# Kernel tuning notes

Hardware: AMD Instinct MI355X
Metric: run time of the kernel (lower is better)

Reference implementation:

```python
import jax, jax.numpy as jnp
import numpy as np

B, N, A = 32, 1024, 256          # batch, n_entities, n_agents
D_IN, D_H, H = 256, 256, 8       # input_dim, hidden_dim, n_heads
SCALE = 1.0 / np.sqrt(D_H)
EPS = 1e-12


def setup_inputs() -> dict:
    key = jax.random.key(0)
    ks = jax.random.split(key, 7)
    x = jax.random.normal(ks[0], (B, N, D_IN), dtype=jnp.float32)
    # binary visibility mask [batch, n_agents, n_entities]
    m = (jax.random.uniform(ks[1], (B, A, N)) > 0.5).astype(jnp.float32)
    # encoder Linear(input_dim, hidden_dim): weight [out,in], bias [out]
    W_enc = jax.random.normal(ks[2], (D_H, D_IN), dtype=jnp.float32) / np.sqrt(D_IN)
    b_enc = jnp.zeros((D_H,), dtype=jnp.float32)
    # per-head projection matrices stacked [H, D_H, D_H] (torch.randn init)
    WQ = jax.random.normal(ks[3], (H, D_H, D_H), dtype=jnp.float32)
    WK = jax.random.normal(ks[4], (H, D_H, D_H), dtype=jnp.float32)
    WV = jax.random.normal(ks[5], (H, D_H, D_H), dtype=jnp.float32)
    return {"x": x, "m": m, "W_enc": W_enc, "b_enc": b_enc, "WQ": WQ, "WK": WK, "WV": WV}


def reference(x, m, W_enc, b_enc, WQ, WK, WV):
    # encode: LeakyReLU then Linear
    h = jnp.einsum('bni,oi->bno', jax.nn.leaky_relu(x), W_enc) + b_enc  # [B,N,D_H]
    n_agents = m.shape[1]
    ha = h[:, :n_agents]                                   # [B,A,D_H]
    # per-head projections, heads vectorized
    Q = jnp.einsum('bad,hde->bhae', ha, WQ)                # [B,H,A,D_H]
    K = jnp.einsum('bnd,hde->bhne', h, WK)                 # [B,H,N,D_H]
    V = jnp.einsum('bnd,hde->bhne', h, WV)                 # [B,H,N,D_H]
    S = jnp.einsum('bhae,bhne->bhan', Q, K) * SCALE        # [B,H,A,N]
    P = jax.nn.softmax(S, axis=-1)
    P = P * m[:, None]                                     # post-softmax mask
    prob = P / (jnp.sum(P, axis=-1, keepdims=True) + EPS)  # renormalize
    z = jnp.einsum('bhan,bhne->bhae', prob, V)             # [B,H,A,D_H]
    return jnp.mean(z, axis=1)                             # [B,A,D_H]
```

## Files before the change

kernel.cpp:

```cpp
#include <hip/hip_runtime.h>
#include <math.h>

namespace {
constexpr int B_N  = 32;
constexpr int SEQ  = 1024;
constexpr int AG   = 256;
constexpr int D    = 256;
constexpr int NH   = 8;
constexpr float SCALE = 0.0625f;
constexpr float EPS   = 1e-12f;

constexpr size_t HHI_OFF  = 0;
constexpr size_t HLO_OFF  = 16777216;
constexpr size_t HT_OFF   = 33554432;
constexpr size_t MTHI_OFF = 50331648;
constexpr size_t MTLO_OFF = 51380224;
constexpr size_t MB_OFF   = 52428800;
constexpr size_t WVT_OFF  = 53477376;
constexpr size_t Z16_OFF  = 54525952;
}

typedef __attribute__((ext_vector_type(8))) short short8;
typedef __attribute__((ext_vector_type(4))) float floatx4;
#define MFMA_BF(A,B,C) __builtin_amdgcn_mfma_f32_16x16x32_bf16(A,B,C,0,0,0)

__device__ __forceinline__ unsigned short bf16_rtne(float f) {
    unsigned u = __float_as_uint(f);
    u += 0x7fffu + ((u >> 16) & 1u);
    return (unsigned short)(u >> 16);
}
__device__ __forceinline__ float bf16_tof(unsigned short h) {
    return __uint_as_float(((unsigned)h) << 16);
}
__device__ __forceinline__ void async16(void* lds, const void* g) {
    __builtin_amdgcn_global_load_lds(
        (const __attribute__((address_space(1))) unsigned int*)g,
        (__attribute__((address_space(3))) unsigned int*)lds,
        16, 0, 0);
}

__global__ __launch_bounds__(256) void enc_kernel(
    const float* __restrict__ x, const float* __restrict__ W_enc,
    const float* __restrict__ b_enc,
    ushort* __restrict__ h_hi, ushort* __restrict__ h_lo)
{
    __shared__ float AsT[32][68];
    __shared__ float BsT[32][68];
    const int t  = threadIdx.x;
    const int tx = t & 15, ty = t >> 4;
    const int col0 = blockIdx.x * 64;
    const int row0 = blockIdx.y * 64;

    float acc[4][4];
#pragma unroll
    for (int r = 0; r < 4; ++r)
#pragma unroll
        for (int c = 0; c < 4; ++c) acc[r][c] = 0.f;

    for (int k0 = 0; k0 < 256; k0 += 32) {
        __syncthreads();
#pragma unroll
        for (int ss = 0; ss < 2; ++ss) {
            int flat = t + 256 * ss;
            int rr = flat >> 3, k4 = flat & 7;
            float4 v = *(const float4*)(x + (size_t)(row0 + rr) * 256 + k0 + k4 * 4);
            v.x = v.x > 0.f ? v.x : 0.01f * v.x;
            v.y = v.y > 0.f ? v.y : 0.01f * v.y;
            v.z = v.z > 0.f ? v.z : 0.01f * v.z;
            v.w = v.w > 0.f ? v.w : 0.01f * v.w;
            AsT[k4*4+0][rr] = v.x; AsT[k4*4+1][rr] = v.y;
            AsT[k4*4+2][rr] = v.z; AsT[k4*4+3][rr] = v.w;
            float4 wv = *(const float4*)(W_enc + (size_t)(col0 + rr) * 256 + k0 + k4 * 4);
            BsT[k4*4+0][rr] = wv.x; BsT[k4*4+1][rr] = wv.y;
            BsT[k4*4+2][rr] = wv.z; BsT[k4*4+3][rr] = wv.w;
        }
        __syncthreads();
#pragma unroll 8
        for (int kk = 0; kk < 32; ++kk) {
            float4 a4 = *(const float4*)&AsT[kk][ty * 4];
            float4 b4 = *(const float4*)&BsT[kk][tx * 4];
            const float ar[4] = {a4.x, a4.y, a4.z, a4.w};
            const float bc[4] = {b4.x, b4.y, b4.z, b4.w};
#pragma unroll
            for (int r = 0; r < 4; ++r)
#pragma unroll
                for (int c = 0; c < 4; ++c)
                    acc[r][c] = fmaf(ar[r], bc[c], acc[r][c]);
        }
    }

    float4 bv = *(const float4*)(b_enc + col0 + tx * 4);
    const float bb4[4] = {bv.x, bv.y, bv.z, bv.w};
#pragma unroll
    for (int r = 0; r < 4; ++r) {
        const int row = row0 + ty * 4 + r;
        ushort hi4[4], lo4[4];
#pragma unroll
        for (int c = 0; c < 4; ++c) {
            float v = acc[r][c] + bb4[c];
            hi4[c] = bf16_rtne(v);
            lo4[c] = bf16_rtne(v - bf16_tof(hi4[c]));
        }
        *(ushort4*)(h_hi + (size_t)row * 256 + col0 + tx * 4) =
            make_ushort4(hi4[0], hi4[1], hi4[2], hi4[3]);
        *(ushort4*)(h_lo + (size_t)row * 256 + col0 + tx * 4) =
            make_ushort4(lo4[0], lo4[1], lo4[2], lo4[3]);
    }
}

__global__ __launch_bounds__(256) void prep_fused(
    const float* __restrict__ m, unsigned* __restrict__ mb,
    const ushort* __restrict__ h_hi, ushort* __restrict__ hT,
    const float* __restrict__ WV, ushort* __restrict__ WVt,
    const float* __restrict__ WQ, const float* __restrict__ WK,
    ushort* __restrict__ Mt_hi, ushort* __restrict__ Mt_lo)
{
    __shared__ __align__(16) char plds[17408];
    const int t = threadIdx.x;
    const int v = blockIdx.x;

    if (v < 1024) {
        const int idx = v * 256 + t;
        const float4* src = (const float4*)(m + (size_t)idx * 32);
        unsigned wbits = 0;
#pragma unroll
        for (int i = 0; i < 8; ++i) {
            float4 vv = src[i];
            wbits |= (vv.x > 0.5f ? 1u : 0u) << (i * 4 + 0);
            wbits |= (vv.y > 0.5f ? 1u : 0u) << (i * 4 + 1);
            wbits |= (vv.z > 0.5f ? 1u : 0u) << (i * 4 + 2);
            wbits |= (vv.w > 0.5f ? 1u : 0u) << (i * 4 + 3);
        }
        mb[idx] = wbits;
    } else if (v < 3072) {
        ushort (*T)[72] = (ushort(*)[72])plds;
        const int v1 = v - 1024;
        const int n0 = (v1 & 15) * 64, d0 = ((v1 >> 4) & 3) * 64, b = v1 >> 6;
        {
            const int r = t >> 2, c = (t & 3) * 16;
            const ushort* src = h_hi + ((size_t)(b * 1024 + n0 + r)) * 256 + d0 + c;
            *(short8*)&T[r][c]     = *(const short8*)src;
            *(short8*)&T[r][c + 8] = *(const short8*)(src + 8);
        }
        __syncthreads();
        {
            const int dd = t >> 2, seg = (t & 3) * 16;
            ushort tmp[16];
#pragma unroll
            for (int j = 0; j < 16; ++j) tmp[j] = T[seg + j][dd];
            ushort* dst = hT + ((size_t)(b * 256 + d0 + dd)) * 1024 + n0 + seg;
            *(short8*)dst       = *(short8*)&tmp[0];
            *(short8*)(dst + 8) = *(short8*)&tmp[8];
        }
    } else if (v < 3200) {
        float (*T)[68] = (float(*)[68])plds;
        const int v2 = v - 3072;
        const int d0 = (v2 & 3) * 64, e0 = ((v2 >> 2) & 3) * 64, h = v2 >> 4;
        {
            const int r = t >> 2, c = (t & 3) * 16;
            const float* src = WV + ((size_t)(h * 256 + d0 + r)) * 256 + e0 + c;
#pragma unroll
            for (int j = 0; j < 4; ++j)
                *(float4*)&T[r][c + j * 4] = *(const float4*)(src + j * 4);
        }
        __syncthreads();
        {
            const int ee = t >> 2, seg = (t & 3) * 16;
            ushort tmp[16];
#pragma unroll
            for (int j = 0; j < 16; ++j) tmp[j] = bf16_rtne(T[seg + j][ee]);
            ushort* dst = WVt + ((size_t)(h * 256 + e0 + ee)) * 256 + d0 + seg;
            *(short8*)dst       = *(short8*)&tmp[0];
            *(short8*)(dst + 8) = *(short8*)&tmp[8];
        }
    } else {
        float (*AsT)[68] = (float(*)[68])plds;
        float (*BsT)[68] = (float(*)[68])(plds + 8704);
        const int v3 = v - 3200;
        const int tx = t & 15, ty = t >> 4;
        const int col0 = (v3 & 3) * 64;
        const int row0 = ((v3 >> 2) & 3) * 64;
        const int hz   = v3 >> 4;
        const float* A  = WK + (size_t)hz * 256 * 256;
        const float* Bm = WQ + (size_t)hz * 256 * 256;
        ushort* Chi = Mt_hi + (size_t)hz * 256 * 256;
        ushort* Clo = Mt_lo + (size_t)hz * 256 * 256;

        float acc[4][4];
#pragma unroll
        for (int r = 0; r < 4; ++r)
#pragma unroll
            for (int c = 0; c < 4; ++c) acc[r][c] = 0.f;

        for (int k0 = 0; k0 < 256; k0 += 32) {
            __syncthreads();
#pragma unroll
            for (int ss = 0; ss < 2; ++ss) {
                int flat = t + 256 * ss;
                int rr = flat >> 3, k4 = flat & 7;
                float4 vv = *(const float4*)(A + (size_t)(row0 + rr) * 256 + k0 + k4 * 4);
                AsT[k4*4+0][rr] = vv.x; AsT[k4*4+1][rr] = vv.y;
                AsT[k4*4+2][rr] = vv.z; AsT[k4*4+3][rr] = vv.w;
                float4 wv = *(const float4*)(Bm + (size_t)(col0 + rr) * 256 + k0 + k4 * 4);
                BsT[k4*4+0][rr] = wv.x; BsT[k4*4+1][rr] = wv.y;
                BsT[k4*4+2][rr] = wv.z; BsT[k4*4+3][rr] = wv.w;
            }
            __syncthreads();
#pragma unroll 8
            for (int kk = 0; kk < 32; ++kk) {
                float4 a4 = *(const float4*)&AsT[kk][ty * 4];
                float4 b4 = *(const float4*)&BsT[kk][tx * 4];
                const float ar[4] = {a4.x, a4.y, a4.z, a4.w};
                const float bc[4] = {b4.x, b4.y, b4.z, b4.w};
#pragma unroll
                for (int r = 0; r < 4; ++r)
#pragma unroll
                    for (int c = 0; c < 4; ++c)
                        acc[r][c] = fmaf(ar[r], bc[c], acc[r][c]);
            }
        }
#pragma unroll
        for (int r = 0; r < 4; ++r) {
            const int row = row0 + ty * 4 + r;
            ushort hi4[4], lo4[4];
#pragma unroll
            for (int c = 0; c < 4; ++c) {
                float vv = acc[r][c];
                hi4[c] = bf16_rtne(vv);
                lo4[c] = bf16_rtne(vv - bf16_tof(hi4[c]));
            }
            *(ushort4*)(Chi + (size_t)row * 256 + col0 + tx * 4) =
                make_ushort4(hi4[0], hi4[1], hi4[2], hi4[3]);
            *(ushort4*)(Clo + (size_t)row * 256 + col0 + tx * 4) =
                make_ushort4(lo4[0], lo4[1], lo4[2], lo4[3]);
        }
    }
}

__global__ __launch_bounds__(512, 2) void attn_mfma(
    const ushort* __restrict__ h_hi, const ushort* __restrict__ h_lo,
    const ushort* __restrict__ hT,   const ushort* __restrict__ Mt_hi,
    const ushort* __restrict__ Mt_lo, const unsigned* __restrict__ mbits,
    ushort* __restrict__ zout)
{
    __shared__ __align__(16) char lds[118784];
    ushort* pP = (ushort*)(lds + 98304);
    ushort* pE = (ushort*)(lds + 108544);

    const int t    = threadIdx.x;
    const int wv   = t >> 6;
    const int lane = t & 63;
    const int l15  = lane & 15;
    const int quad = lane >> 4;
    const int f    = blockIdx.x;
    const int b    = (f & 7) + 8 * (f >> 7);
    const int mid  = (f >> 3) & 15;
    const int hh   = (mid >> 2) * 2 + (wv >> 2);
    const int a0   = (mid & 3) * 64;
    const int aw   = a0 + (wv & 3) * 16;

    const ushort* hbh = h_hi + (size_t)b * SEQ * D;
    const ushort* hbl = h_lo + (size_t)b * SEQ * D;
    const ushort* hTb = hT   + (size_t)b * D * SEQ;

    floatx4 qac[16];
#pragma unroll
    for (int i = 0; i < 16; ++i) qac[i] = (floatx4){0.f, 0.f, 0.f, 0.f};

    for (int kc = 0; kc < 4; ++kc) {
        short8 Ah[2], Al[2];
#pragma unroll
        for (int kt = 0; kt < 2; ++kt) {
            const size_t ao = ((size_t)b * SEQ + aw + l15) * D +
                              kc * 64 + kt * 32 + quad * 8;
            Ah[kt] = *(const short8*)(h_hi + ao);
            Al[kt] = *(const short8*)(h_lo + ao);
        }
#pragma unroll
        for (int nt2 = 0; nt2 < 16; ++nt2) {
#pragma unroll
            for (int kt = 0; kt < 2; ++kt) {
                const size_t mo = ((size_t)hh * D + nt2 * 16 + l15) * D +
                                  kc * 64 + kt * 32 + quad * 8;
                short8 Bh = *(const short8*)(Mt_hi + mo);
                short8 Bl = *(const short8*)(Mt_lo + mo);
                qac[nt2] = MFMA_BF(Ah[kt], Bh, qac[nt2]);
                qac[nt2] = MFMA_BF(Al[kt], Bh, qac[nt2]);
                qac[nt2] = MFMA_BF(Ah[kt], Bl, qac[nt2]);
            }
        }
    }

    short8 Qhi[8], Qlo[8];
    {
        float* qscr = (float*)lds;
        for (int c = 0; c < 4; ++c) {
#pragma unroll
            for (int j = 0; j < 4; ++j)
#pragma unroll
                for (int r = 0; r < 4; ++r)
                    qscr[(wv * 16 + quad * 4 + r) * 68 + j * 16 + l15] = qac[c * 4 + j][r];
#pragma unroll
            for (int kt = 0; kt < 2; ++kt) {
                const float* pr = &qscr[(wv * 16 + l15) * 68 + kt * 32 + quad * 8];
                float ftmp[8];
                *(float4*)&ftmp[0] = *(const float4*)pr;
                *(float4*)&ftmp[4] = *(const float4*)(pr + 4);
                short8 hi, lo;
#pragma unroll
                for (int e = 0; e < 8; ++e) {
                    unsigned short hb = bf16_rtne(ftmp[e]);
                    hi[e] = (short)hb;
                    lo[e] = (short)bf16_rtne(ftmp[e] - bf16_tof(hb));
                }
                Qhi[c * 2 + kt] = hi;
                Qlo[c * 2 + kt] = lo;
            }
        }
    }
    __syncthreads();

    auto issue_tile = [&](char* buf, int n0) {
        ushort* dh = (ushort*)buf;
        ushort* dl = (ushort*)(buf + 16384);
        ushort* dT = (ushort*)(buf + 32768);
#pragma unroll
        for (int i = 0; i < 2; ++i) {
            const int slot = wv * 128 + i * 64 + lane;
            const int row  = slot >> 5;
            const int p    = slot & 31;
            const int c    = p ^ (row & 7);
            const size_t go = (size_t)(n0 + row) * 256 + c * 8;
            const size_t lo_ = (size_t)(wv * 128 + i * 64) * 8;
            async16(dh + lo_, hbh + go);
            async16(dl + lo_, hbl + go);
        }
#pragma unroll
        for (int i = 0; i < 2; ++i) {
            const int slot = wv * 128 + i * 64 + lane;
            const int row  = slot >> 2;
            const int p    = slot & 3;
            const int c    = p ^ ((row >> 2) & 3);
            async16(dT + (size_t)(wv * 128 + i * 64) * 8,
                    hTb + (size_t)row * 1024 + n0 + c * 8);
        }
    };

    issue_tile(lds,         0);
    issue_tile(lds + 49152, 32);
    __syncthreads();

    floatx4 zac[16];
#pragma unroll
    for (int i = 0; i < 16; ++i) zac[i] = (floatx4){0.f, 0.f, 0.f, 0.f};
    floatx4 zacZ = (floatx4){0.f, 0.f, 0.f, 0.f};
    floatx4 zacE = (floatx4){0.f, 0.f, 0.f, 0.f};
    float mx[4] = {-INFINITY, -INFINITY, -INFINITY, -INFINITY};

    short8 onesf;
#pragma unroll
    for (int e = 0; e < 8; ++e) onesf[e] = (short)0x3F80;

    const unsigned* mbr = mbits + ((size_t)b * AG + aw + quad * 4) * (SEQ / 32);

    for (int nt = 0; nt < 32; ++nt) {
        char* cur = lds + (size_t)(nt & 1) * 49152;
        ushort* hS_hi = (ushort*)cur;
        ushort* hS_lo = (ushort*)(cur + 16384);
        ushort* hTS   = (ushort*)(cur + 32768);

        floatx4 sacH[2], sacL[2];
        sacH[0] = (floatx4){0.f, 0.f, 0.f, 0.f};
        sacH[1] = (floatx4){0.f, 0.f, 0.f, 0.f};
        sacL[0] = (floatx4){0.f, 0.f, 0.f, 0.f};
        sacL[1] = (floatx4){0.f, 0.f, 0.f, 0.f};
#pragma unroll
        for (int ks = 0; ks < 8; ++ks) {
            const int cg = ks * 4 + quad;
#pragma unroll
            for (int ntile = 0; ntile < 2; ++ntile) {
                const int row = ntile * 16 + l15;
                const int off = row * 256 + (cg ^ (row & 7)) * 8;
                short8 Bh = *(const short8*)&hS_hi[off];
                short8 Bl = *(const short8*)&hS_lo[off];
                sacH[ntile] = MFMA_BF(Qhi[ks], Bh, sacH[ntile]);
                sacL[ntile] = MFMA_BF(Qlo[ks], Bh, sacL[ntile]);
                sacL[ntile] = MFMA_BF(Qhi[ks], Bl, sacL[ntile]);
            }
        }

        float l0[4], l1[4];
#pragma unroll
        for (int r = 0; r < 4; ++r) {
            l0[r] = (sacH[0][r] + sacL[0][r]) * SCALE;
            l1[r] = (sacH[1][r] + sacL[1][r]) * SCALE;
        }

        float mt[4];
#pragma unroll
        for (int r = 0; r < 4; ++r) mt[r] = fmaxf(l0[r], l1[r]);
#pragma unroll
        for (int off = 1; off < 16; off <<= 1) {
#pragma unroll
            for (int r = 0; r < 4; ++r)
                mt[r] = fmaxf(mt[r], __shfl_xor(mt[r], off));
        }

        const bool need = (mt[0] > mx[0] + 8.0f) || (mt[1] > mx[1] + 8.0f) ||
                          (mt[2] > mx[2] + 8.0f) || (mt[3] > mx[3] + 8.0f);
        if (__any(need)) {
            float alr[4];
#pragma unroll
            for (int r = 0; r < 4; ++r) {
                const float mxn = fmaxf(mx[r], mt[r]);
                alr[r] = __expf(mx[r] - mxn);
                mx[r] = mxn;
            }
#pragma unroll
            for (int dt = 0; dt < 16; ++dt) {
                zac[dt][0] *= alr[0]; zac[dt][1] *= alr[1];
                zac[dt][2] *= alr[2]; zac[dt][3] *= alr[3];
            }
            zacZ[0] *= alr[0]; zacZ[1] *= alr[1];
            zacZ[2] *= alr[2]; zacZ[3] *= alr[3];
            zacE[0] *= alr[0]; zacE[1] *= alr[1];
            zacE[2] *= alr[2]; zacE[3] *= alr[3];
        }

#pragma unroll
        for (int r = 0; r < 4; ++r) {
            const unsigned w0 = mbr[r * (SEQ / 32) + nt];
            const float e0 = __expf(l0[r] - mx[r]);
            const float e1 = __expf(l1[r] - mx[r]);
            const float p0 = ((w0 >> l15) & 1u)        ? e0 : 0.f;
            const float p1 = ((w0 >> (16 + l15)) & 1u) ? e1 : 0.f;
            const int row = wv * 16 + quad * 4 + r;
            pP[row * 40 + l15]      = bf16_rtne(p0);
            pP[row * 40 + 16 + l15] = bf16_rtne(p1);
            pE[row * 40 + l15]      = bf16_rtne(e0);
            pE[row * 40 + 16 + l15] = bf16_rtne(e1);
        }

        short8 Pf = *(const short8*)&pP[(wv * 16 + l15) * 40 + quad * 8];
        short8 Ef = *(const short8*)&pE[(wv * 16 + l15) * 40 + quad * 8];
        zacZ = MFMA_BF(Pf, onesf, zacZ);
        zacE = MFMA_BF(Ef, onesf, zacE);

#pragma unroll
        for (int dt = 0; dt < 16; ++dt) {
            const int row = dt * 16 + l15;
            const int p   = quad ^ ((row >> 2) & 3);
            short8 Bf = *(const short8*)&hTS[row * 32 + p * 8];
            zac[dt] = MFMA_BF(Pf, Bf, zac[dt]);
        }

        __syncthreads();
        if (nt + 2 < 32) issue_tile(cur, (nt + 2) * 32);
    }

#pragma unroll
    for (int r = 0; r < 4; ++r) {
        const int a = aw + quad * 4 + r;
        const float inv = 1.0f / (zacZ[r] + EPS * zacE[r]);
        ushort* zr = zout + (((size_t)b * NH + hh) * AG + a) * D;
#pragma unroll
        for (int dt = 0; dt < 16; ++dt)
            zr[dt * 16 + l15] = bf16_rtne(zac[dt][r] * inv);
    }
}

__global__ __launch_bounds__(256) void out_mfma(
    const ushort* __restrict__ z16, const ushort* __restrict__ WVt,
    float* __restrict__ out)
{
    const int t    = threadIdx.x;
    const int wv   = t >> 6;
    const int lane = t & 63;
    const int l15  = lane & 15;
    const int quad = lane >> 4;
    const int e0 = blockIdx.x * 64;
    const int a0 = blockIdx.y * 64;
    const int b  = blockIdx.z;
    const int aw = a0 + wv * 16;

    floatx4 acc[4];
#pragma unroll
    for (int i = 0; i < 4; ++i) acc[i] = (floatx4){0.f, 0.f, 0.f, 0.f};

#pragma unroll 4
    for (int c = 0; c < 64; ++c) {
        const int hh = c >> 3, d0 = (c & 7) * 32;
        short8 Af = *(const short8*)(z16 +
            (((size_t)b * NH + hh) * AG + aw + l15) * D + d0 + quad * 8);
#pragma unroll
        for (int et = 0; et < 4; ++et) {
            short8 Bf = *(const short8*)(WVt +
                ((size_t)hh * D + e0 + et * 16 + l15) * D + d0 + quad * 8);
            acc[et] = MFMA_BF(Af, Bf, acc[et]);
        }
    }
#pragma unroll
    for (int et = 0; et < 4; ++et)
#pragma unroll
        for (int r = 0; r < 4; ++r)
            out[((size_t)b * AG + aw + quad * 4 + r) * D + e0 + et * 16 + l15] =
                acc[et][r] * 0.125f;
}

extern "C" void kernel_launch(void* const* d_in, const int* in_sizes, int n_in,
                              void* d_out, int out_size, void* d_ws, size_t ws_size,
                              hipStream_t stream)
{
    (void)in_sizes; (void)n_in; (void)out_size; (void)ws_size;
    const float* x     = (const float*)d_in[0];
    const float* m     = (const float*)d_in[1];
    const float* W_enc = (const float*)d_in[2];
    const float* b_enc = (const float*)d_in[3];
    const float* WQ    = (const float*)d_in[4];
    const float* WK    = (const float*)d_in[5];
    const float* WV    = (const float*)d_in[6];
    float* out = (float*)d_out;
    char* ws = (char*)d_ws;

    ushort*   h_hi  = (ushort*)(ws + HHI_OFF);
    ushort*   h_lo  = (ushort*)(ws + HLO_OFF);
    ushort*   hT    = (ushort*)(ws + HT_OFF);
    ushort*   Mt_hi = (ushort*)(ws + MTHI_OFF);
    ushort*   Mt_lo = (ushort*)(ws + MTLO_OFF);
    unsigned* mbits = (unsigned*)(ws + MB_OFF);
    ushort*   WVt   = (ushort*)(ws + WVT_OFF);
    ushort*   z16   = (ushort*)(ws + Z16_OFF);

    enc_kernel<<<dim3(4, 512, 1), dim3(256), 0, stream>>>(
        x, W_enc, b_enc, h_hi, h_lo);
    prep_fused<<<dim3(3328, 1, 1), dim3(256), 0, stream>>>(
        m, mbits, h_hi, hT, WV, WVt, WQ, WK, Mt_hi, Mt_lo);
    attn_mfma<<<dim3(512, 1, 1), dim3(512), 0, stream>>>(
        h_hi, h_lo, hT, Mt_hi, Mt_lo, mbits, z16);
    out_mfma<<<dim3(4, 4, B_N), dim3(256), 0, stream>>>(z16, WVt, out);
}
```

Measured before the change: 550.9 us.

## Triple-buffer attention tiles and compute next tile's scores one iteration ahead

Moves the LDS ring for K/V tiles from two buffers to three and software-pipelines the QK^T score MFMAs. Each iteration now computes the scores for tile nt+1 while tile nt goes through softmax, masking and PV accumulation, and it issues the async load for tile nt+2 at the start of the iteration. The P/E staging buffer is placed in the consumed hi-half of the current tile, and the score MFMAs run under a raised wave priority. The aim is to hide load latency and the softmax dependency chain behind MFMA work, at the cost of more LDS and more live registers.

```diff
diff --git a/kernel.cpp b/kernel.cpp
--- a/kernel.cpp
+++ b/kernel.cpp
@@ -243,9 +243,8 @@
     const ushort* __restrict__ Mt_lo, const unsigned* __restrict__ mbits,
     ushort* __restrict__ zout)
 {
-    __shared__ __align__(16) char lds[118784];
-    ushort* pP = (ushort*)(lds + 98304);
-    ushort* pE = (ushort*)(lds + 108544);
+    __shared__ __align__(16) char lds[157696];
+    ushort* pP = (ushort*)(lds + 147456);
 
     const int t    = threadIdx.x;
     const int wv   = t >> 6;
@@ -346,34 +345,14 @@
         }
     };
 
-    issue_tile(lds,         0);
-    issue_tile(lds + 49152, 32);
-    __syncthreads();
-
-    floatx4 zac[16];
-#pragma unroll
-    for (int i = 0; i < 16; ++i) zac[i] = (floatx4){0.f, 0.f, 0.f, 0.f};
-    floatx4 zacZ = (floatx4){0.f, 0.f, 0.f, 0.f};
-    floatx4 zacE = (floatx4){0.f, 0.f, 0.f, 0.f};
-    float mx[4] = {-INFINITY, -INFINITY, -INFINITY, -INFINITY};
-
-    short8 onesf;
-#pragma unroll
-    for (int e = 0; e < 8; ++e) onesf[e] = (short)0x3F80;
-
-    const unsigned* mbr = mbits + ((size_t)b * AG + aw + quad * 4) * (SEQ / 32);
-
-    for (int nt = 0; nt < 32; ++nt) {
-        char* cur = lds + (size_t)(nt & 1) * 49152;
-        ushort* hS_hi = (ushort*)cur;
-        ushort* hS_lo = (ushort*)(cur + 16384);
-        ushort* hTS   = (ushort*)(cur + 32768);
-
-        floatx4 sacH[2], sacL[2];
-        sacH[0] = (floatx4){0.f, 0.f, 0.f, 0.f};
-        sacH[1] = (floatx4){0.f, 0.f, 0.f, 0.f};
-        sacL[0] = (floatx4){0.f, 0.f, 0.f, 0.f};
-        sacL[1] = (floatx4){0.f, 0.f, 0.f, 0.f};
+    auto compute_S = [&](char* buf, floatx4* sH, floatx4* sL) {
+        ushort* hS_hi = (ushort*)buf;
+        ushort* hS_lo = (ushort*)(buf + 16384);
+        sH[0] = (floatx4){0.f, 0.f, 0.f, 0.f};
+        sH[1] = (floatx4){0.f, 0.f, 0.f, 0.f};
+        sL[0] = (floatx4){0.f, 0.f, 0.f, 0.f};
+        sL[1] = (floatx4){0.f, 0.f, 0.f, 0.f};
+        __builtin_amdgcn_s_setprio(1);
 #pragma unroll
         for (int ks = 0; ks < 8; ++ks) {
             const int cg = ks * 4 + quad;
@@ -383,10 +362,46 @@
                 const int off = row * 256 + (cg ^ (row & 7)) * 8;
                 short8 Bh = *(const short8*)&hS_hi[off];
                 short8 Bl = *(const short8*)&hS_lo[off];
-                sacH[ntile] = MFMA_BF(Qhi[ks], Bh, sacH[ntile]);
-                sacL[ntile] = MFMA_BF(Qlo[ks], Bh, sacL[ntile]);
-                sacL[ntile] = MFMA_BF(Qhi[ks], Bl, sacL[ntile]);
-            }
+                sH[ntile] = MFMA_BF(Qhi[ks], Bh, sH[ntile]);
+                sL[ntile] = MFMA_BF(Qlo[ks], Bh, sL[ntile]);
+                sL[ntile] = MFMA_BF(Qhi[ks], Bl, sL[ntile]);
+            }
+        }
+        __builtin_amdgcn_s_setprio(0);
+    };
+
+    char* bufA = lds;
+    char* bufB = lds + 49152;
+    char* bufC = lds + 98304;
+    issue_tile(bufA, 0);
+    issue_tile(bufB, 32);
+    __syncthreads();
+
+    floatx4 zac[16];
+#pragma unroll
+    for (int i = 0; i < 16; ++i) zac[i] = (floatx4){0.f, 0.f, 0.f, 0.f};
+    floatx4 zacZ = (floatx4){0.f, 0.f, 0.f, 0.f};
+    floatx4 zacE = (floatx4){0.f, 0.f, 0.f, 0.f};
+    float mx[4] = {-INFINITY, -INFINITY, -INFINITY, -INFINITY};
+
+    short8 onesf;
+#pragma unroll
+    for (int e = 0; e < 8; ++e) onesf[e] = (short)0x3F80;
+
+    const unsigned* mbr = mbits + ((size_t)b * AG + aw + quad * 4) * (SEQ / 32);
+
+    floatx4 sacH[2], sacL[2];
+    compute_S(bufA, sacH, sacL);
+    __syncthreads();
+
+    for (int nt = 0; nt < 32; ++nt) {
+        if (nt + 2 < 32) issue_tile(bufC, (nt + 2) * 32);
+
+        floatx4 nsH[2], nsL[2];
+        if (nt + 1 < 32) {
+            compute_S(bufB, nsH, nsL);
+        } else {
+            nsH[0] = nsH[1] = nsL[0] = nsL[1] = (floatx4){0.f, 0.f, 0.f, 0.f};
         }
 
         float l0[4], l1[4];
@@ -427,6 +442,7 @@
             zacE[2] *= alr[2]; zacE[3] *= alr[3];
         }
 
+        ushort* pE = (ushort*)bufA;
 #pragma unroll
         for (int r = 0; r < 4; ++r) {
             const unsigned w0 = mbr[r * (SEQ / 32) + nt];
@@ -446,6 +462,7 @@
         zacZ = MFMA_BF(Pf, onesf, zacZ);
         zacE = MFMA_BF(Ef, onesf, zacE);
 
+        ushort* hTS = (ushort*)(bufA + 32768);
 #pragma unroll
         for (int dt = 0; dt < 16; ++dt) {
             const int row = dt * 16 + l15;
@@ -455,7 +472,10 @@
         }
 
         __syncthreads();
-        if (nt + 2 < 32) issue_tile(cur, (nt + 2) * 32);
+
+        char* tmp = bufA; bufA = bufB; bufB = bufC; bufC = tmp;
+        sacH[0] = nsH[0]; sacH[1] = nsH[1];
+        sacL[0] = nsL[0]; sacL[1] = nsL[1];
     }
 
 #pragma unroll
```

Result: no change. 555.3 us (+0.8%).

## Move encoder GEMM to split-bf16 MFMA and fuse h transpose into encoder

Applied to the files above, without the earlier changes.

The encoder Linear layer used to be an FP32 scalar-FMA tiled GEMM. It now runs on bf16 MFMA with a three-term hi/lo split that keeps close to FP32 accuracy. The epilogue stages the result in LDS and also writes the transposed hT directly, so the separate transpose blocks are dropped from prep_fused and h_hi is no longer re-read from global memory. This costs extra bf16 conversion work on load and more LDS per block. The encoder is only one part of the total time, which limits the overall effect.

```diff
diff --git a/kernel.cpp b/kernel.cpp
--- a/kernel.cpp
+++ b/kernel.cpp
@@ -39,78 +39,109 @@
         16, 0, 0);
 }
 
-__global__ __launch_bounds__(256) void enc_kernel(
+__global__ __launch_bounds__(256) void enc_mfma(
     const float* __restrict__ x, const float* __restrict__ W_enc,
     const float* __restrict__ b_enc,
-    ushort* __restrict__ h_hi, ushort* __restrict__ h_lo)
+    ushort* __restrict__ h_hi, ushort* __restrict__ h_lo,
+    ushort* __restrict__ hT)
 {
-    __shared__ float AsT[32][68];
-    __shared__ float BsT[32][68];
-    const int t  = threadIdx.x;
-    const int tx = t & 15, ty = t >> 4;
+    __shared__ ushort Ah[64][40], Al[64][40];
+    __shared__ ushort Bh[64][40], Bl[64][40];
+    __shared__ ushort Th[64][72], Tl[64][72];
+
+    const int t    = threadIdx.x;
+    const int wv   = t >> 6;
+    const int lane = t & 63;
+    const int l15  = lane & 15;
+    const int quad = lane >> 4;
     const int col0 = blockIdx.x * 64;
     const int row0 = blockIdx.y * 64;
 
-    float acc[4][4];
-#pragma unroll
-    for (int r = 0; r < 4; ++r)
-#pragma unroll
-        for (int c = 0; c < 4; ++c) acc[r][c] = 0.f;
+    floatx4 acc[4];
+#pragma unroll
+    for (int i = 0; i < 4; ++i) acc[i] = (floatx4){0.f, 0.f, 0.f, 0.f};
 
     for (int k0 = 0; k0 < 256; k0 += 32) {
         __syncthreads();
-#pragma unroll
-        for (int ss = 0; ss < 2; ++ss) {
-            int flat = t + 256 * ss;
-            int rr = flat >> 3, k4 = flat & 7;
-            float4 v = *(const float4*)(x + (size_t)(row0 + rr) * 256 + k0 + k4 * 4);
-            v.x = v.x > 0.f ? v.x : 0.01f * v.x;
-            v.y = v.y > 0.f ? v.y : 0.01f * v.y;
-            v.z = v.z > 0.f ? v.z : 0.01f * v.z;
-            v.w = v.w > 0.f ? v.w : 0.01f * v.w;
-            AsT[k4*4+0][rr] = v.x; AsT[k4*4+1][rr] = v.y;
-            AsT[k4*4+2][rr] = v.z; AsT[k4*4+3][rr] = v.w;
-            float4 wv = *(const float4*)(W_enc + (size_t)(col0 + rr) * 256 + k0 + k4 * 4);
-            BsT[k4*4+0][rr] = wv.x; BsT[k4*4+1][rr] = wv.y;
-            BsT[k4*4+2][rr] = wv.z; BsT[k4*4+3][rr] = wv.w;
+        {
+            const int r = t >> 2, s = (t & 3) * 8;
+            float f[8];
+            *(float4*)&f[0] = *(const float4*)(x + (size_t)(row0 + r) * 256 + k0 + s);
+            *(float4*)&f[4] = *(const float4*)(x + (size_t)(row0 + r) * 256 + k0 + s + 4);
+            short8 hi8, lo8;
+#pragma unroll
+            for (int e = 0; e < 8; ++e) {
+                float v = f[e] > 0.f ? f[e] : 0.01f * f[e];
+                unsigned short hb = bf16_rtne(v);
+                hi8[e] = (short)hb;
+                lo8[e] = (short)bf16_rtne(v - bf16_tof(hb));
+            }
+            *(short8*)&Ah[r][s] = hi8;
+            *(short8*)&Al[r][s] = lo8;
+            *(float4*)&f[0] = *(const float4*)(W_enc + (size_t)(col0 + r) * 256 + k0 + s);
+            *(float4*)&f[4] = *(const float4*)(W_enc + (size_t)(col0 + r) * 256 + k0 + s + 4);
+#pragma unroll
+            for (int e = 0; e < 8; ++e) {
+                unsigned short hb = bf16_rtne(f[e]);
+                hi8[e] = (short)hb;
+                lo8[e] = (short)bf16_rtne(f[e] - bf16_tof(hb));
+            }
+            *(short8*)&Bh[r][s] = hi8;
+            *(short8*)&Bl[r][s] = lo8;
         }
         __syncthreads();
-#pragma unroll 8
-        for (int kk = 0; kk < 32; ++kk) {
-            float4 a4 = *(const float4*)&AsT[kk][ty * 4];
-            float4 b4 = *(const float4*)&BsT[kk][tx * 4];
-            const float ar[4] = {a4.x, a4.y, a4.z, a4.w};
-            const float bc[4] = {b4.x, b4.y, b4.z, b4.w};
-#pragma unroll
-            for (int r = 0; r < 4; ++r)
-#pragma unroll
-                for (int c = 0; c < 4; ++c)
-                    acc[r][c] = fmaf(ar[r], bc[c], acc[r][c]);
-        }
-    }
-
-    float4 bv = *(const float4*)(b_enc + col0 + tx * 4);
-    const float bb4[4] = {bv.x, bv.y, bv.z, bv.w};
-#pragma unroll
-    for (int r = 0; r < 4; ++r) {
-        const int row = row0 + ty * 4 + r;
-        ushort hi4[4], lo4[4];
-#pragma unroll
-        for (int c = 0; c < 4; ++c) {
-            float v = acc[r][c] + bb4[c];
-            hi4[c] = bf16_rtne(v);
-            lo4[c] = bf16_rtne(v - bf16_tof(hi4[c]));
-        }
-        *(ushort4*)(h_hi + (size_t)row * 256 + col0 + tx * 4) =
-            make_ushort4(hi4[0], hi4[1], hi4[2], hi4[3]);
-        *(ushort4*)(h_lo + (size_t)row * 256 + col0 + tx * 4) =
-            make_ushort4(lo4[0], lo4[1], lo4[2], lo4[3]);
+
+        short8 Af  = *(const short8*)&Ah[wv * 16 + l15][quad * 8];
+        short8 Afl = *(const short8*)&Al[wv * 16 + l15][quad * 8];
+#pragma unroll
+        for (int et = 0; et < 4; ++et) {
+            short8 Bf  = *(const short8*)&Bh[et * 16 + l15][quad * 8];
+            short8 Bfl = *(const short8*)&Bl[et * 16 + l15][quad * 8];
+            acc[et] = MFMA_BF(Af,  Bf,  acc[et]);
+            acc[et] = MFMA_BF(Afl, Bf,  acc[et]);
+            acc[et] = MFMA_BF(Af,  Bfl, acc[et]);
+        }
+    }
+
+    __syncthreads();
+#pragma unroll
+    for (int et = 0; et < 4; ++et) {
+        const int col = et * 16 + l15;
+        const float bb = b_enc[col0 + col];
+#pragma unroll
+        for (int r = 0; r < 4; ++r) {
+            const int row = wv * 16 + quad * 4 + r;
+            const float v = acc[et][r] + bb;
+            const unsigned short hb = bf16_rtne(v);
+            Th[row][col] = hb;
+            Tl[row][col] = bf16_rtne(v - bf16_tof(hb));
+        }
+    }
+    __syncthreads();
+    {
+        const int r = t >> 2, c0 = (t & 3) * 16;
+        ushort* dh = h_hi + (size_t)(row0 + r) * 256 + col0 + c0;
+        ushort* dl = h_lo + (size_t)(row0 + r) * 256 + col0 + c0;
+        *(short8*)dh       = *(const short8*)&Th[r][c0];
+        *(short8*)(dh + 8) = *(const short8*)&Th[r][c0 + 8];
+        *(short8*)dl       = *(const short8*)&Tl[r][c0];
+        *(short8*)(dl + 8) = *(const short8*)&Tl[r][c0 + 8];
+    }
+    {
+        const int bq = (int)blockIdx.y >> 4;
+        const int n0 = ((int)blockIdx.y & 15) * 64;
+        const int dd = t >> 2, seg = (t & 3) * 16;
+        ushort tmp[16];
+#pragma unroll
+        for (int j = 0; j < 16; ++j) tmp[j] = Th[seg + j][dd];
+        ushort* dst = hT + ((size_t)(bq * 256 + col0 + dd)) * 1024 + n0 + seg;
+        *(short8*)dst       = *(short8*)&tmp[0];
+        *(short8*)(dst + 8) = *(short8*)&tmp[8];
     }
 }
 
 __global__ __launch_bounds__(256) void prep_fused(
     const float* __restrict__ m, unsigned* __restrict__ mb,
-    const ushort* __restrict__ h_hi, ushort* __restrict__ hT,
     const float* __restrict__ WV, ushort* __restrict__ WVt,
     const float* __restrict__ WQ, const float* __restrict__ WK,
     ushort* __restrict__ Mt_hi, ushort* __restrict__ Mt_lo)
@@ -132,29 +163,9 @@
             wbits |= (vv.w > 0.5f ? 1u : 0u) << (i * 4 + 3);
         }
         mb[idx] = wbits;
-    } else if (v < 3072) {
-        ushort (*T)[72] = (ushort(*)[72])plds;
-        const int v1 = v - 1024;
-        const int n0 = (v1 & 15) * 64, d0 = ((v1 >> 4) & 3) * 64, b = v1 >> 6;
-        {
-            const int r = t >> 2, c = (t & 3) * 16;
-            const ushort* src = h_hi + ((size_t)(b * 1024 + n0 + r)) * 256 + d0 + c;
-            *(short8*)&T[r][c]     = *(const short8*)src;
-            *(short8*)&T[r][c + 8] = *(const short8*)(src + 8);
-        }
-        __syncthreads();
-        {
-            const int dd = t >> 2, seg = (t & 3) * 16;
-            ushort tmp[16];
-#pragma unroll
-            for (int j = 0; j < 16; ++j) tmp[j] = T[seg + j][dd];
-            ushort* dst = hT + ((size_t)(b * 256 + d0 + dd)) * 1024 + n0 + seg;
-            *(short8*)dst       = *(short8*)&tmp[0];
-            *(short8*)(dst + 8) = *(short8*)&tmp[8];
-        }
-    } else if (v < 3200) {
+    } else if (v < 1152) {
         float (*T)[68] = (float(*)[68])plds;
-        const int v2 = v - 3072;
+        const int v2 = v - 1024;
         const int d0 = (v2 & 3) * 64, e0 = ((v2 >> 2) & 3) * 64, h = v2 >> 4;
         {
             const int r = t >> 2, c = (t & 3) * 16;
@@ -176,7 +187,7 @@
     } else {
         float (*AsT)[68] = (float(*)[68])plds;
         float (*BsT)[68] = (float(*)[68])(plds + 8704);
-        const int v3 = v - 3200;
+        const int v3 = v - 1152;
         const int tx = t & 15, ty = t >> 4;
         const int col0 = (v3 & 3) * 64;
         const int row0 = ((v3 >> 2) & 3) * 64;
@@ -531,10 +542,10 @@
     ushort*   WVt   = (ushort*)(ws + WVT_OFF);
     ushort*   z16   = (ushort*)(ws + Z16_OFF);
 
-    enc_kernel<<<dim3(4, 512, 1), dim3(256), 0, stream>>>(
-        x, W_enc, b_enc, h_hi, h_lo);
-    prep_fused<<<dim3(3328, 1, 1), dim3(256), 0, stream>>>(
-        m, mbits, h_hi, hT, WV, WVt, WQ, WK, Mt_hi, Mt_lo);
+    enc_mfma<<<dim3(4, 512, 1), dim3(256), 0, stream>>>(
+        x, W_enc, b_enc, h_hi, h_lo, hT);
+    prep_fused<<<dim3(1280, 1, 1), dim3(256), 0, stream>>>(
+        m, mbits, WV, WVt, WQ, WK, Mt_hi, Mt_lo);
     attn_mfma<<<dim3(512, 1, 1), dim3(512), 0, stream>>>(
         h_hi, h_lo, hT, Mt_hi, Mt_lo, mbits, z16);
     out_mfma<<<dim3(4, 4, B_N), dim3(256), 0, stream>>>(z16, WVt, out);
```

Measured after the change: 528.8 us. 4.0% less time.
